# Optimization experiments

Measured on AMD Instinct MI355X. Metric: run time of the kernel, lower is better.

## Reference

```python
import jax, jax.numpy as jnp
import numpy as np

N = 8192       # nodes
IN_F = 512     # in_features
OUT_F = 256    # out_features


def setup_inputs() -> dict:
    key = jax.random.key(0)
    k1, k2, k3, k4 = jax.random.split(key, 4)
    # xavier_uniform-like scales for params
    w_scale = 1.414 * (6.0 / (IN_F + OUT_F)) ** 0.5
    a_scale = 1.414 * (6.0 / (2 * OUT_F + 1)) ** 0.5
    x = jax.random.normal(k1, (N, IN_F), jnp.float32)
    W = jax.random.uniform(k2, (IN_F, OUT_F), jnp.float32, -w_scale, w_scale)
    a = jax.random.uniform(k3, (2 * OUT_F, 1), jnp.float32, -a_scale, a_scale)
    adj = jax.random.randint(k4, (N, N), 0, 2, jnp.int32)
    return {"x": x, "W": W, "a": a, "adj": adj}


def reference(x, W, a, adj):
    # h = x @ W : [N, OUT_F]
    h = x @ W
    f = W.shape[1]
    a1, a2 = a[:f], a[f:]          # each [OUT_F, 1]
    # Original builds a_input[i,j] = concat(h_i, h_j) then matmuls with a.
    # Equivalent decomposition: e[i,j] = h_i . a1 + h_j . a2
    e = (h @ a1) + (h @ a2).T      # [N, N]
    neg = jnp.float32(-9e15)
    attention = jnp.where(adj > 0, e, neg)   # no softmax in the original
    h_prime = attention @ h        # [N, OUT_F]
    return h_prime
```

## Files before the change

### kernel.cpp

```cpp
#include <hip/hip_runtime.h>


#define NEG_BIG (-9000000000000000.0f)
#define POS_BIG (9000000000000000.0f)

typedef __bf16 bf16x8 __attribute__((ext_vector_type(8)));
typedef float f32x16 __attribute__((ext_vector_type(16)));

static __device__ __forceinline__ unsigned short f2bf(float f) {
  unsigned u = __builtin_bit_cast(unsigned, f);
  u = u + 0x7FFFu + ((u >> 16) & 1u);
  return (unsigned short)(u >> 16);
}
static __device__ __forceinline__ float bfbits2f(unsigned hi16) {
  return __builtin_bit_cast(float, hi16 << 16);
}
static __device__ __forceinline__ unsigned pk2(float a, float b) {
  return (unsigned)f2bf(a) | ((unsigned)f2bf(b) << 16);
}
static __device__ __forceinline__ bf16x8 asbf(int4 q) {
  return __builtin_bit_cast(bf16x8, q);
}
static __device__ __forceinline__ f32x16 mfma(bf16x8 a, int4 b, f32x16 c) {
  return __builtin_amdgcn_mfma_f32_32x32x16_bf16(a, asbf(b), c, 0, 0, 0);
}
static __device__ __forceinline__ bf16x8 expand8(unsigned b) {
  union { unsigned w[4]; bf16x8 f; } r;
  r.w[0] = ((b & 1u)        | ((b & 2u)   << 15)) * 0x3F80u;
  r.w[1] = (((b >> 2) & 1u) | ((b & 8u)   << 13)) * 0x3F80u;
  r.w[2] = (((b >> 4) & 1u) | ((b & 32u)  << 11)) * 0x3F80u;
  r.w[3] = (((b >> 6) & 1u) | ((b & 128u) << 9))  * 0x3F80u;
  return r.f;
}

__global__ __launch_bounds__(256, 2) void k0_bits(const int* __restrict__ adj,
                                                  unsigned char* __restrict__ bitT) {
  __shared__ unsigned char LT[1024 * 20];
  const int t = threadIdx.x;
  const int rb = blockIdx.x;
  const int* base = adj + (size_t)rb * 16 * 8192 + t * 32;
  unsigned c[4] = {0u, 0u, 0u, 0u};
#pragma unroll
  for (int rr = 0; rr < 16; ++rr) {
    const int4* p = (const int4*)(base + (size_t)rr * 8192);
    int4 q[8];
#pragma unroll
    for (int k = 0; k < 8; ++k) q[k] = p[k];
#pragma unroll
    for (int i = 0; i < 4; ++i) {
      int4 u = q[2 * i], v = q[2 * i + 1];
      unsigned by = (u.x & 1) | ((u.y & 1) << 1) | ((u.z & 1) << 2) | ((u.w & 1) << 3)
                  | ((v.x & 1) << 4) | ((v.y & 1) << 5) | ((v.z & 1) << 6) | ((v.w & 1) << 7);
      c[i] |= by << ((rr & 3) * 8);
    }
    if ((rr & 3) == 3) {
#pragma unroll
      for (int i = 0; i < 4; ++i) {
        *(unsigned*)&LT[(t * 4 + i) * 20 + (rr & ~3)] = c[i];
        c[i] = 0u;
      }
    }
  }
  __syncthreads();
#pragma unroll
  for (int jc = 0; jc < 4; ++jc) {
    const int j8 = jc * 256 + t;
    int4 v;
    v.x = *(const int*)&LT[j8 * 20];
    v.y = *(const int*)&LT[j8 * 20 + 4];
    v.z = *(const int*)&LT[j8 * 20 + 8];
    v.w = *(const int*)&LT[j8 * 20 + 12];
    *(int4*)(bitT + (size_t)j8 * 8192 + rb * 16) = v;
  }
}

__global__ void k1a_wt(const float* __restrict__ W, unsigned short* __restrict__ WT,
                       float* __restrict__ T) {
  const int i = blockIdx.x * 256 + threadIdx.x;
  const int k = i >> 8, n = i & 255;
  WT[n * 512 + k] = f2bf(W[i]);
  if (blockIdx.x == 0) T[threadIdx.x] = 0.f;
}

__global__ __launch_bounds__(256) void k1b_h(const float* __restrict__ x,
    const unsigned short* __restrict__ WT, unsigned short* __restrict__ hP) {
  __shared__ unsigned short XS[64 * 264];
  const int t = threadIdx.x;
  const int mt = blockIdx.x;
  const int m0 = mt << 5;
  const int row = t >> 3, c7 = t & 7;
  const float* xr = x + (size_t)(m0 + row) * 512 + c7 * 4;
  const int gb = c7 >> 1, off = (t & 1) * 4;
#pragma unroll
  for (int j = 0; j < 16; ++j) {
    float4 v = *(const float4*)(xr + 32 * j);
    *(uint2*)&XS[(gb + 4 * j) * 264 + row * 8 + off] =
        make_uint2(pk2(v.x, v.y), pk2(v.z, v.w));
  }
  __syncthreads();
  const int w = t >> 6, l = t & 63, l31 = l & 31, lh = l >> 5;
  f32x16 acc0, acc1;
  for (int i = 0; i < 16; ++i) { acc0[i] = 0.f; acc1[i] = 0.f; }
  const int nt0 = w * 2;
  const unsigned short* w0 = WT + (size_t)(nt0 * 32 + l31) * 512 + lh * 8;
  const unsigned short* w1 = w0 + 32 * 512;
  const char* XB = (const char*)XS + lh * 528 + l31 * 16;
#pragma unroll 4
  for (int ks = 0; ks < 32; ++ks) {
    bf16x8 Af = *(const bf16x8*)(XB + ks * 1056);
    int4 b0 = *(const int4*)(w0 + ks * 16);
    int4 b1 = *(const int4*)(w1 + ks * 16);
    acc0 = mfma(Af, b0, acc0);
    acc1 = mfma(Af, b1, acc1);
  }
#pragma unroll
  for (int reg = 0; reg < 16; ++reg) {
    const int mm = (reg & 3) + 8 * (reg >> 2) + 4 * lh;
    hP[(size_t)mt * 8192 + (nt0 * 32 + l31) * 32 + mm] = f2bf(acc0[reg]);
    hP[(size_t)mt * 8192 + ((nt0 + 1) * 32 + l31) * 32 + mm] = f2bf(acc1[reg]);
  }
}

__global__ __launch_bounds__(256) void k2_colsum(const unsigned short* __restrict__ hP,
                                                 float* __restrict__ T) {
  const int t = threadIdx.x;
  const int b = blockIdx.x;
  const int4* p = (const int4*)(hP + (size_t)b * 8192 + t * 32);
  int4 q0 = p[0], q1 = p[1], q2 = p[2], q3 = p[3];
  float s = 0.f;
  const unsigned* u0 = (const unsigned*)&q0;
  const unsigned* u1 = (const unsigned*)&q1;
  const unsigned* u2 = (const unsigned*)&q2;
  const unsigned* u3 = (const unsigned*)&q3;
#pragma unroll
  for (int i = 0; i < 4; ++i) {
    s += bfbits2f(u0[i] & 0xFFFFu) + bfbits2f(u0[i] >> 16);
    s += bfbits2f(u1[i] & 0xFFFFu) + bfbits2f(u1[i] >> 16);
    s += bfbits2f(u2[i] & 0xFFFFu) + bfbits2f(u2[i] >> 16);
    s += bfbits2f(u3[i] & 0xFFFFu) + bfbits2f(u3[i] >> 16);
  }
  atomicAdd(&T[t], s);
}

__global__ void k2b_init(const float* __restrict__ T, float* __restrict__ out) {
  const int i = blockIdx.x * 256 + threadIdx.x;
  const int n4 = (i & 63) * 4;
  float4 tv = *(const float4*)(T + n4);
  float4 o;
  o.x = NEG_BIG * tv.x; o.y = NEG_BIG * tv.y;
  o.z = NEG_BIG * tv.z; o.w = NEG_BIG * tv.w;
  ((float4*)out)[i] = o;
}

template<int MODE>
__global__ __launch_bounds__(256, 2) void k3_att(const unsigned char* __restrict__ bitT,
    const unsigned short* __restrict__ hP, float* __restrict__ outp) {
  const int t = threadIdx.x, blk = blockIdx.x;
  const int s = blk & 7;
  const int rg = blk >> 3;
  const int w = t >> 6, l = t & 63, l31 = l & 31, lh = l >> 5;
  const int rt = rg * 2 + (w >> 1);
  const int nh = w & 1;

  const unsigned char* bq = bitT + (size_t)(s * 128 + lh) * 8192 + rt * 64 + l31;
  const unsigned short* hB = hP + (size_t)(s * 32) * 8192
                              + (size_t)(nh * 128 + l31) * 32 + lh * 8;

  f32x16 acc[2][4];
#pragma unroll
  for (int mt = 0; mt < 2; ++mt)
#pragma unroll
    for (int nt = 0; nt < 4; ++nt)
#pragma unroll
      for (int i = 0; i < 16; ++i) acc[mt][nt][i] = 0.f;

  int4 Bv[8];
  unsigned cb[4], nb[4];

#define BYTELOAD(dst, it)                                                   \
  _Pragma("unroll")                                                         \
  for (int mk = 0; mk < 4; ++mk)                                            \
    dst[mk] = bq[(size_t)((it) * 4 + (mk & 1) * 2) * 8192 + (mk >> 1) * 32];
#define BLOAD(it)                                                           \
  {                                                                         \
    const unsigned short* hb = hB + (size_t)(it) * 8192;                    \
    _Pragma("unroll")                                                       \
    for (int ks = 0; ks < 2; ++ks)                                          \
      _Pragma("unroll")                                                     \
      for (int nt = 0; nt < 4; ++nt)                                        \
        Bv[ks * 4 + nt] = *(const int4*)(hb + nt * 1024 + ks * 16);         \
  }

  BYTELOAD(cb, 0)

#pragma unroll 1
  for (int it = 0; it < 32; ++it) {
    BLOAD(it)
    if (it + 1 < 32) { BYTELOAD(nb, it + 1) }
#pragma unroll
    for (int ks = 0; ks < 2; ++ks) {
      bf16x8 A0 = expand8(cb[ks]);
      bf16x8 A1 = expand8(cb[2 + ks]);
#pragma unroll
      for (int nt = 0; nt < 4; ++nt) {
        acc[0][nt] = mfma(A0, Bv[ks * 4 + nt], acc[0][nt]);
        acc[1][nt] = mfma(A1, Bv[ks * 4 + nt], acc[1][nt]);
      }
    }
#pragma unroll
    for (int mk = 0; mk < 4; ++mk) cb[mk] = nb[mk];
  }
#undef BYTELOAD
#undef BLOAD

#pragma unroll
  for (int mt = 0; mt < 2; ++mt)
#pragma unroll
    for (int nt = 0; nt < 4; ++nt) {
      const int nn = nh * 128 + nt * 32 + l31;
#pragma unroll
      for (int reg = 0; reg < 16; ++reg) {
        const int rr = rt * 64 + mt * 32 + (reg & 3) + 8 * (reg >> 2) + 4 * lh;
        if (MODE == 0) {
          outp[(size_t)s * 2097152 + (size_t)rr * 256 + nn] = acc[mt][nt][reg];
        } else {
          atomicAdd(outp + (size_t)rr * 256 + nn, POS_BIG * acc[mt][nt][reg]);
        }
      }
    }
}

__global__ __launch_bounds__(256) void k4_reduce(const float* __restrict__ P,
    const float* __restrict__ T, float* __restrict__ out) {
  const int i = blockIdx.x * 256 + threadIdx.x;
  float4 tv = *(const float4*)(T + (i & 63) * 4);
  const float4* P4 = (const float4*)P;
  float sx = 0.f, sy = 0.f, sz = 0.f, sw = 0.f;
#pragma unroll
  for (int sp = 0; sp < 8; ++sp) {
    float4 v = P4[(size_t)sp * 524288 + i];
    sx += v.x; sy += v.y; sz += v.z; sw += v.w;
  }
  float4 o;
  o.x = POS_BIG * sx + NEG_BIG * tv.x;
  o.y = POS_BIG * sy + NEG_BIG * tv.y;
  o.z = POS_BIG * sz + NEG_BIG * tv.z;
  o.w = POS_BIG * sw + NEG_BIG * tv.w;
  ((float4*)out)[i] = o;
}

extern "C" void kernel_launch(void* const* d_in, const int* in_sizes, int n_in,
                              void* d_out, int out_size, void* d_ws, size_t ws_size,
                              hipStream_t stream) {
  const float* x = (const float*)d_in[0];
  const float* W = (const float*)d_in[1];
  const int* adj = (const int*)d_in[3];
  float* out = (float*)d_out;
  char* ws = (char*)d_ws;
  unsigned short* WT = (unsigned short*)(ws);
  unsigned short* hP = (unsigned short*)(ws + (1 << 20));
  float* T = (float*)(ws + (6 << 20));
  unsigned char* bitT = (unsigned char*)(ws + (16 << 20));
  float* P = (float*)(ws + (32 << 20));

  const bool fit = ws_size >= ((size_t)(32 << 20) + (size_t)64 * 1024 * 1024);

  k0_bits<<<512, 256, 0, stream>>>(adj, bitT);
  k1a_wt<<<512, 256, 0, stream>>>(W, WT, T);
  k1b_h<<<256, 256, 0, stream>>>(x, WT, hP);
  k2_colsum<<<256, 256, 0, stream>>>(hP, T);
  if (fit) {
    k3_att<0><<<512, 256, 0, stream>>>(bitT, hP, P);
    k4_reduce<<<2048, 256, 0, stream>>>(P, T, out);
  } else {
    k2b_init<<<2048, 256, 0, stream>>>(T, out);
    k3_att<1><<<512, 256, 0, stream>>>(bitT, hP, out);
  }
}
```

Measured before the change: 525.7 us.

## Store adjacency bits row-major and shrink attention tiles for more blocks

The bit-packing kernel now writes the adjacency bitmask row-major with one word per thread per row, dropping the shared-memory transpose and the block barrier. The attention kernel reads 16-byte bit chunks per row, extracts bytes with shifts, and gives each wave a single 32-column output tile with two row accumulators. This raises the block count to 2048 and the occupancy hint to 4. It aims to cut register pressure and make the adjacency loads coalesced, at the cost of reloading h more often and running more blocks.

```diff
diff --git a/kernel.cpp b/kernel.cpp
--- a/kernel.cpp
+++ b/kernel.cpp
@@ -33,44 +33,26 @@
   return r.f;
 }
 
-__global__ __launch_bounds__(256, 2) void k0_bits(const int* __restrict__ adj,
-                                                  unsigned char* __restrict__ bitT) {
-  __shared__ unsigned char LT[1024 * 20];
-  const int t = threadIdx.x;
-  const int rb = blockIdx.x;
-  const int* base = adj + (size_t)rb * 16 * 8192 + t * 32;
-  unsigned c[4] = {0u, 0u, 0u, 0u};
-#pragma unroll
-  for (int rr = 0; rr < 16; ++rr) {
+__global__ __launch_bounds__(256) void k0_bits(const int* __restrict__ adj,
+                                               unsigned char* __restrict__ bitB) {
+  const int t = threadIdx.x, rb = blockIdx.x;
+  const int* base = adj + (size_t)rb * 4 * 8192 + t * 32;
+  unsigned* outw = (unsigned*)(bitB + (size_t)rb * 4 * 1024 + t * 4);
+#pragma unroll 2
+  for (int rr = 0; rr < 4; ++rr) {
     const int4* p = (const int4*)(base + (size_t)rr * 8192);
     int4 q[8];
 #pragma unroll
     for (int k = 0; k < 8; ++k) q[k] = p[k];
+    unsigned word = 0;
 #pragma unroll
     for (int i = 0; i < 4; ++i) {
       int4 u = q[2 * i], v = q[2 * i + 1];
       unsigned by = (u.x & 1) | ((u.y & 1) << 1) | ((u.z & 1) << 2) | ((u.w & 1) << 3)
                   | ((v.x & 1) << 4) | ((v.y & 1) << 5) | ((v.z & 1) << 6) | ((v.w & 1) << 7);
-      c[i] |= by << ((rr & 3) * 8);
+      word |= by << (8 * i);
     }
-    if ((rr & 3) == 3) {
-#pragma unroll
-      for (int i = 0; i < 4; ++i) {
-        *(unsigned*)&LT[(t * 4 + i) * 20 + (rr & ~3)] = c[i];
-        c[i] = 0u;
-      }
-    }
-  }
-  __syncthreads();
-#pragma unroll
-  for (int jc = 0; jc < 4; ++jc) {
-    const int j8 = jc * 256 + t;
-    int4 v;
-    v.x = *(const int*)&LT[j8 * 20];
-    v.y = *(const int*)&LT[j8 * 20 + 4];
-    v.z = *(const int*)&LT[j8 * 20 + 8];
-    v.w = *(const int*)&LT[j8 * 20 + 12];
-    *(int4*)(bitT + (size_t)j8 * 8192 + rb * 16) = v;
+    outw[rr * 256] = word;
   }
 }
 
@@ -153,81 +135,63 @@
 }
 
 template<int MODE>
-__global__ __launch_bounds__(256, 2) void k3_att(const unsigned char* __restrict__ bitT,
+__global__ __launch_bounds__(256, 4) void k3_att(const unsigned char* __restrict__ bitB,
     const unsigned short* __restrict__ hP, float* __restrict__ outp) {
   const int t = threadIdx.x, blk = blockIdx.x;
   const int s = blk & 7;
-  const int rg = blk >> 3;
+  const int g = blk >> 3;
+  const int rt = g >> 1;
   const int w = t >> 6, l = t & 63, l31 = l & 31, lh = l >> 5;
-  const int rt = rg * 2 + (w >> 1);
-  const int nh = w & 1;
-
-  const unsigned char* bq = bitT + (size_t)(s * 128 + lh) * 8192 + rt * 64 + l31;
+  const int nt = (g & 1) * 4 + w;
+  const int R0 = rt * 64;
+
+  const unsigned char* bp0 = bitB + (size_t)(R0 + l31) * 1024 + s * 128;
+  const unsigned char* bp1 = bp0 + (size_t)32 * 1024;
   const unsigned short* hB = hP + (size_t)(s * 32) * 8192
-                              + (size_t)(nh * 128 + l31) * 32 + lh * 8;
-
-  f32x16 acc[2][4];
-#pragma unroll
-  for (int mt = 0; mt < 2; ++mt)
-#pragma unroll
-    for (int nt = 0; nt < 4; ++nt)
-#pragma unroll
-      for (int i = 0; i < 16; ++i) acc[mt][nt][i] = 0.f;
-
-  int4 Bv[8];
-  unsigned cb[4], nb[4];
-
-#define BYTELOAD(dst, it)                                                   \
-  _Pragma("unroll")                                                         \
-  for (int mk = 0; mk < 4; ++mk)                                            \
-    dst[mk] = bq[(size_t)((it) * 4 + (mk & 1) * 2) * 8192 + (mk >> 1) * 32];
-#define BLOAD(it)                                                           \
-  {                                                                         \
-    const unsigned short* hb = hB + (size_t)(it) * 8192;                    \
-    _Pragma("unroll")                                                       \
-    for (int ks = 0; ks < 2; ++ks)                                          \
-      _Pragma("unroll")                                                     \
-      for (int nt = 0; nt < 4; ++nt)                                        \
-        Bv[ks * 4 + nt] = *(const int4*)(hb + nt * 1024 + ks * 16);         \
-  }
-
-  BYTELOAD(cb, 0)
+                              + (size_t)(nt * 32 + l31) * 32 + lh * 8;
+  const unsigned shl = lh * 8, shh = shl + 16;
+
+  f32x16 acc0, acc1;
+#pragma unroll
+  for (int i = 0; i < 16; ++i) { acc0[i] = 0.f; acc1[i] = 0.f; }
 
 #pragma unroll 1
-  for (int it = 0; it < 32; ++it) {
-    BLOAD(it)
-    if (it + 1 < 32) { BYTELOAD(nb, it + 1) }
-#pragma unroll
-    for (int ks = 0; ks < 2; ++ks) {
-      bf16x8 A0 = expand8(cb[ks]);
-      bf16x8 A1 = expand8(cb[2 + ks]);
-#pragma unroll
-      for (int nt = 0; nt < 4; ++nt) {
-        acc[0][nt] = mfma(A0, Bv[ks * 4 + nt], acc[0][nt]);
-        acc[1][nt] = mfma(A1, Bv[ks * 4 + nt], acc[1][nt]);
+  for (int gi = 0; gi < 8; ++gi) {
+    int4 w0 = *(const int4*)(bp0 + gi * 16);
+    int4 w1 = *(const int4*)(bp1 + gi * 16);
+    const unsigned* u0 = (const unsigned*)&w0;
+    const unsigned* u1 = (const unsigned*)&w1;
+#pragma unroll
+    for (int q = 0; q < 4; ++q) {
+      const unsigned short* hb = hB + (size_t)(gi * 4 + q) * 8192;
+      int4 bv0 = *(const int4*)(hb);
+      int4 bv1 = *(const int4*)(hb + 16);
+      const unsigned d0 = u0[q], d1 = u1[q];
+      bf16x8 A00 = expand8((d0 >> shl) & 255u);
+      bf16x8 A01 = expand8((d0 >> shh) & 255u);
+      bf16x8 A10 = expand8((d1 >> shl) & 255u);
+      bf16x8 A11 = expand8((d1 >> shh) & 255u);
+      acc0 = mfma(A00, bv0, acc0);
+      acc1 = mfma(A10, bv0, acc1);
+      acc0 = mfma(A01, bv1, acc0);
+      acc1 = mfma(A11, bv1, acc1);
+    }
+  }
+
+  const int nn = nt * 32 + l31;
+#pragma unroll
+  for (int mt = 0; mt < 2; ++mt) {
+    const f32x16& a = mt ? acc1 : acc0;
+#pragma unroll
+    for (int reg = 0; reg < 16; ++reg) {
+      const int rr = R0 + mt * 32 + (reg & 3) + 8 * (reg >> 2) + 4 * lh;
+      if (MODE == 0) {
+        outp[(size_t)s * 2097152 + (size_t)rr * 256 + nn] = a[reg];
+      } else {
+        atomicAdd(outp + (size_t)rr * 256 + nn, POS_BIG * a[reg]);
       }
     }
-#pragma unroll
-    for (int mk = 0; mk < 4; ++mk) cb[mk] = nb[mk];
-  }
-#undef BYTELOAD
-#undef BLOAD
-
-#pragma unroll
-  for (int mt = 0; mt < 2; ++mt)
-#pragma unroll
-    for (int nt = 0; nt < 4; ++nt) {
-      const int nn = nh * 128 + nt * 32 + l31;
-#pragma unroll
-      for (int reg = 0; reg < 16; ++reg) {
-        const int rr = rt * 64 + mt * 32 + (reg & 3) + 8 * (reg >> 2) + 4 * lh;
-        if (MODE == 0) {
-          outp[(size_t)s * 2097152 + (size_t)rr * 256 + nn] = acc[mt][nt][reg];
-        } else {
-          atomicAdd(outp + (size_t)rr * 256 + nn, POS_BIG * acc[mt][nt][reg]);
-        }
-      }
-    }
+  }
 }
 
 __global__ __launch_bounds__(256) void k4_reduce(const float* __restrict__ P,
@@ -260,20 +224,20 @@
   unsigned short* WT = (unsigned short*)(ws);
   unsigned short* hP = (unsigned short*)(ws + (1 << 20));
   float* T = (float*)(ws + (6 << 20));
-  unsigned char* bitT = (unsigned char*)(ws + (16 << 20));
+  unsigned char* bitB = (unsigned char*)(ws + (16 << 20));
   float* P = (float*)(ws + (32 << 20));
 
   const bool fit = ws_size >= ((size_t)(32 << 20) + (size_t)64 * 1024 * 1024);
 
-  k0_bits<<<512, 256, 0, stream>>>(adj, bitT);
+  k0_bits<<<2048, 256, 0, stream>>>(adj, bitB);
   k1a_wt<<<512, 256, 0, stream>>>(W, WT, T);
   k1b_h<<<256, 256, 0, stream>>>(x, WT, hP);
   k2_colsum<<<256, 256, 0, stream>>>(hP, T);
   if (fit) {
-    k3_att<0><<<512, 256, 0, stream>>>(bitT, hP, P);
+    k3_att<0><<<2048, 256, 0, stream>>>(bitB, hP, P);
     k4_reduce<<<2048, 256, 0, stream>>>(P, T, out);
   } else {
     k2b_init<<<2048, 256, 0, stream>>>(T, out);
-    k3_att<1><<<512, 256, 0, stream>>>(bitT, hP, out);
-  }
-}
+    k3_att<1><<<2048, 256, 0, stream>>>(bitB, hP, out);
+  }
+}
```

New measurement: 473.6 us. 9.9% less time.
